# Performance work log

Hardware: AMD Instinct MI355X
Metric: run time of the kernel (lower is better)

The kernel has to match this reference:

```python
import jax, jax.numpy as jnp
import numpy as np

H, DQK, DV, DM, POS = 8, 64, 64, 768, 64

def _rel_basis(l, n):
    # Enformer central-mask relative position basis: [l, l, n]
    pos = jnp.arange(l)
    distance = pos[None, :] - pos[:, None]              # [l, l] int
    half = n // 2
    pow_rate = jnp.exp(jnp.log(jnp.asarray((l + 1) / 2.0, jnp.float32)) / half)
    center_widths = pow_rate ** jnp.arange(1, half + 1, dtype=jnp.float32)  # [half]
    unsigned = (jnp.abs(distance)[:, :, None].astype(jnp.float32) <= center_widths)
    signed = jnp.sign(distance)[:, :, None] * unsigned
    return jnp.concatenate([unsigned.astype(jnp.float32), signed.astype(jnp.float32)], axis=-1)

def setup_inputs() -> dict:
    key = jax.random.key(0)
    ks = jax.random.split(key, 9)
    b, l = 2, 1024
    x = jax.random.normal(ks[0], (b, l, DM), jnp.float32)
    # torch Linear weights: [out, in]
    Wq = jax.random.normal(ks[1], (H * DQK, DM), jnp.float32) * (1.0 / np.sqrt(DM))
    Wk = jax.random.normal(ks[2], (H * DQK, DM), jnp.float32) * (1.0 / np.sqrt(DM))
    Wv = jax.random.normal(ks[3], (H * DV, DM), jnp.float32) * (1.0 / np.sqrt(DM))
    Wo = jax.random.normal(ks[4], (DM, H * DV), jnp.float32) * (1.0 / np.sqrt(H * DV))
    bo = jnp.zeros((DM,), jnp.float32)
    u_bias = jax.random.normal(ks[5], (H, DQK), jnp.float32) * np.sqrt(2.0 / DQK)
    v_bias = jax.random.normal(ks[6], (H, DQK), jnp.float32) * np.sqrt(2.0 / DQK)
    w_pos = jax.random.normal(ks[7], (H, DQK, POS), jnp.float32) * np.sqrt(2.0 / POS)
    return {"x": x, "Wq": Wq, "Wk": Wk, "Wv": Wv, "Wo": Wo, "bo": bo,
            "u_bias": u_bias, "v_bias": v_bias, "w_pos": w_pos}

def reference(x, Wq, Wk, Wv, Wo, bo, u_bias, v_bias, w_pos):
    b, l, _ = x.shape
    q = (x @ Wq.T).reshape(b, l, H, DQK)
    k = (x @ Wk.T).reshape(b, l, H, DQK)
    v = (x @ Wv.T).reshape(b, l, H, DV)
    basis = _rel_basis(l, POS)                           # [l, l, n]
    scale = 1.0 / np.sqrt(DQK)
    # qr_term: einsum('bihd,hdn,ijn->bhij') factored to avoid [b,h,l,l,d]
    qw = jnp.einsum('bihd,hdn->bhin', q, w_pos)          # [b,h,l,n]
    qr = jnp.einsum('bhin,ijn->bhij', qw, basis)
    uk = jnp.einsum('hd,bjhd->bhj', u_bias, k)[:, :, None, :]
    vw = jnp.einsum('hd,hdn->hn', v_bias, w_pos)
    vr = jnp.einsum('hn,ijn->hij', vw, basis)[None]      # [1,h,l,l]
    bias = (qr + uk + vr) * scale
    scores = jnp.einsum('bihd,bjhd->bhij', q, k) * scale + bias
    attn = jax.nn.softmax(scores, axis=-1)
    out = jnp.einsum('bhij,bjhd->bihd', attn, v).reshape(b, l, H * DV)
    return out @ Wo.T + bo
```

## Files before the change

### kernel.cpp

```cpp
#include <hip/hip_runtime.h>

#define LSEQ 1024
#define NB   2
#define NH   8
#define DD   64
#define DMOD 768

using bf16x8 = __attribute__((ext_vector_type(8))) short;
using f32x4  = __attribute__((ext_vector_type(4))) float;

__device__ inline unsigned short f2bf(float f) {
    union { float f; unsigned u; } v; v.f = f;
    unsigned r = v.u + 0x7FFFu + ((v.u >> 16) & 1u);
    return (unsigned short)(r >> 16);
}
__device__ inline float bf2f(unsigned short u) {
    union { unsigned u; float f; } v; v.u = ((unsigned)u) << 16;
    return v.f;
}

__global__ __launch_bounds__(256) void pack_all(
    const float4* __restrict__ x,  const float4* __restrict__ wq,
    const float4* __restrict__ wk, const float4* __restrict__ wv,
    const float4* __restrict__ wo,
    ushort4* __restrict__ xb, ushort4* __restrict__ wqb, ushort4* __restrict__ wkb,
    ushort4* __restrict__ wvb, ushort4* __restrict__ wob)
{
    int i = blockIdx.x * 256 + threadIdx.x;
    const float4* src; ushort4* dst; int off;
    if (i < 393216)      { src = x;  dst = xb;  off = i; }
    else if (i < 491520) { src = wq; dst = wqb; off = i - 393216; }
    else if (i < 589824) { src = wk; dst = wkb; off = i - 491520; }
    else if (i < 688128) { src = wv; dst = wvb; off = i - 589824; }
    else                 { src = wo; dst = wob; off = i - 688128; }
    float4 v = src[off];
    ushort4 o;
    o.x = f2bf(v.x); o.y = f2bf(v.y); o.z = f2bf(v.z); o.w = f2bf(v.w);
    dst[off] = o;
}

__global__ void setup_kernel(const float* __restrict__ v_bias,
                             const float* __restrict__ w_pos,
                             float* __restrict__ vsfx,
                             unsigned char* __restrict__ cls_g)
{
    __shared__ float w_s[32];
    __shared__ float vw_s[8][64];
    __shared__ int cmin_s[1024];
    int tid = threadIdx.x;
    if (tid < 32) {
        float pr = expf(logf(512.5f) / 32.0f);
        w_s[tid] = powf(pr, (float)(tid + 1));
    }
    __syncthreads();
    for (int d = tid; d < 1024; d += 256) {
        float fd = (float)d;
        int cm = 32;
        for (int c = 31; c >= 0; --c) if (fd <= w_s[c]) cm = c;
        cmin_s[d] = cm;
    }
    for (int idx = tid; idx < 512; idx += 256) {
        int hh = idx >> 6, n = idx & 63;
        float s = 0.f;
        for (int d = 0; d < 64; ++d)
            s += v_bias[hh * 64 + d] * w_pos[(hh * 64 + d) * 64 + n];
        vw_s[hh][n] = s;
    }
    __syncthreads();
    for (int idx = tid; idx < 512; idx += 256) {
        int hh = idx >> 6, n = idx & 63;
        float s = 0.f;
        if (n < 32) { for (int c = n;      c < 32; ++c) s += vw_s[hh][c]; }
        else        { for (int c = n - 32; c < 32; ++c) s += vw_s[hh][32 + c]; }
        vsfx[idx] = s;
    }
    for (int d2 = tid; d2 < 2048; d2 += 256) {
        int dd = d2 - 1023;
        int ad = dd < 0 ? -dd : dd; if (ad > 1023) ad = 1023;
        int t = (dd < 0) ? 0 : ((dd == 0) ? 1 : 2);
        cls_g[d2] = (unsigned char)(t * 33 + cmin_s[ad]);
    }
}

__global__ __launch_bounds__(256) void gemm_qkv(
    const unsigned short* __restrict__ X, const unsigned short* __restrict__ W,
    const float* __restrict__ ub,
    unsigned short* __restrict__ Qb, unsigned short* __restrict__ Kb,
    unsigned short* __restrict__ Vtb)
{
    __shared__ unsigned short Xs[64][40];
    __shared__ unsigned short Wsm[64][40];
    __shared__ unsigned short Ct[64][72];

    int tid = threadIdx.x;
    int w = tid >> 6, lane = tid & 63, l15 = lane & 15, q = lane >> 4;
    int M0 = blockIdx.y * 64, N0 = blockIdx.x * 64;
    int rs = tid >> 2, seg = tid & 3;

    f32x4 acc[4] = {};
    for (int k0 = 0; k0 < 768; k0 += 32) {
        uint4 xv = *(const uint4*)(X + (size_t)(M0 + rs) * 768 + k0 + seg * 8);
        uint4 wv = *(const uint4*)(W + (size_t)(N0 + rs) * 768 + k0 + seg * 8);
        *(uint4*)&Xs[rs][seg * 8]  = xv;
        *(uint4*)&Wsm[rs][seg * 8] = wv;
        __syncthreads();
        bf16x8 a = *(bf16x8*)&Xs[w * 16 + l15][q * 8];
#pragma unroll
        for (int ct = 0; ct < 4; ++ct) {
            bf16x8 bfr = *(bf16x8*)&Wsm[ct * 16 + l15][q * 8];
            acc[ct] = __builtin_amdgcn_mfma_f32_16x16x32_bf16(a, bfr, acc[ct], 0, 0, 0);
        }
        __syncthreads();
    }

    if (N0 < 1024) {
        int isQ = (N0 < 512);
#pragma unroll
        for (int ct = 0; ct < 4; ++ct) {
            float u0 = isQ ? ub[N0 + ct * 16 + l15] : 0.f;
            float sc = isQ ? 0.125f : 1.0f;
#pragma unroll
            for (int r = 0; r < 4; ++r)
                Ct[w * 16 + q * 4 + r][ct * 16 + l15] = f2bf((acc[ct][r] + u0) * sc);
        }
        __syncthreads();
        int Nh = isQ ? N0 : (N0 - 512);
        unsigned short* out = isQ ? Qb : Kb;
        size_t base = ((size_t)((M0 >> 10) * 8 + (Nh >> 6)) * 1024 + (M0 & 1023)) * 64;
#pragma unroll
        for (int it = 0; it < 2; ++it) {
            int idx = tid + it * 256;
            int row = idx >> 3, sg = idx & 7;
            *(uint4*)(out + base + (size_t)row * 64 + sg * 8) = *(uint4*)&Ct[row][sg * 8];
        }
    } else {
#pragma unroll
        for (int ct = 0; ct < 4; ++ct) {
            ushort4 pk;
            pk.x = f2bf(acc[ct][0]); pk.y = f2bf(acc[ct][1]);
            pk.z = f2bf(acc[ct][2]); pk.w = f2bf(acc[ct][3]);
            *(ushort4*)&Ct[ct * 16 + l15][w * 16 + q * 4] = pk;
        }
        __syncthreads();
        size_t base = ((size_t)((M0 >> 10) * 8 + ((N0 - 1024) >> 6))) * 65536;
        int j0 = M0 & 1023;
#pragma unroll
        for (int it = 0; it < 2; ++it) {
            int idx = tid + it * 256;
            int d = idx >> 3, sg = idx & 7;
            *(uint4*)(Vtb + base + (size_t)d * 1024 + j0 + sg * 8) = *(uint4*)&Ct[d][sg * 8];
        }
    }
}

__global__ __launch_bounds__(256) void gemm_o(
    const unsigned short* __restrict__ X, const unsigned short* __restrict__ W,
    const float* __restrict__ bias, float* __restrict__ out)
{
    __shared__ unsigned short Xs[64][40];
    __shared__ unsigned short Wsm[64][40];
    __shared__ float Ctf[64][72];

    int tid = threadIdx.x;
    int w = tid >> 6, lane = tid & 63, l15 = lane & 15, q = lane >> 4;
    int M0 = blockIdx.y * 64, N0 = blockIdx.x * 64;
    int rs = tid >> 2, seg = tid & 3;

    f32x4 acc[4] = {};
    for (int k0 = 0; k0 < 512; k0 += 32) {
        uint4 xv = *(const uint4*)(X + (size_t)(M0 + rs) * 512 + k0 + seg * 8);
        uint4 wv = *(const uint4*)(W + (size_t)(N0 + rs) * 512 + k0 + seg * 8);
        *(uint4*)&Xs[rs][seg * 8]  = xv;
        *(uint4*)&Wsm[rs][seg * 8] = wv;
        __syncthreads();
        bf16x8 a = *(bf16x8*)&Xs[w * 16 + l15][q * 8];
#pragma unroll
        for (int ct = 0; ct < 4; ++ct) {
            bf16x8 bfr = *(bf16x8*)&Wsm[ct * 16 + l15][q * 8];
            acc[ct] = __builtin_amdgcn_mfma_f32_16x16x32_bf16(a, bfr, acc[ct], 0, 0, 0);
        }
        __syncthreads();
    }
#pragma unroll
    for (int ct = 0; ct < 4; ++ct) {
        float bv = bias[N0 + ct * 16 + l15];
#pragma unroll
        for (int r = 0; r < 4; ++r)
            Ctf[w * 16 + q * 4 + r][ct * 16 + l15] = acc[ct][r] + bv;
    }
    __syncthreads();
#pragma unroll
    for (int it = 0; it < 4; ++it) {
        int idx = tid + it * 256;
        int row = idx >> 4, sg = idx & 15;
        *(float4*)(out + (size_t)(M0 + row) * 768 + N0 + sg * 4) = *(float4*)&Ctf[row][sg * 4];
    }
}

__global__ __launch_bounds__(256) void qw_sfx_kernel(
    const unsigned short* __restrict__ qb,
    const float* __restrict__ w_pos,
    const float* __restrict__ ub,
    float* __restrict__ qsfx)
{
    __shared__ float wps[64][64];
    __shared__ float qs[4][64];
    __shared__ float qw[4][64];
    int h = blockIdx.y, b = blockIdx.z;
    int i0 = blockIdx.x * 4;
    int n = threadIdx.x, r = threadIdx.y;
    int tid = r * 64 + n;
    for (int idx = tid; idx < 4096; idx += 256)
        wps[idx >> 6][idx & 63] = w_pos[h * 4096 + idx];
    qs[r][n] = bf2f(qb[((size_t)(b * 8 + h) * 1024 + i0 + r) * 64 + n]) * 8.0f
               - ub[h * 64 + n];
    __syncthreads();
    float acc = 0.f;
#pragma unroll 8
    for (int d = 0; d < 64; ++d) acc += qs[r][d] * wps[d][n];
    qw[r][n] = acc;
    __syncthreads();
    float s = 0.f;
    if (n < 32) { for (int c = 31; c >= n;      --c) s += qw[r][c]; }
    else        { for (int c = 31; c >= n - 32; --c) s += qw[r][32 + c]; }
    qsfx[((size_t)(b * 8 + h) * 1024 + i0 + r) * 64 + n] = s;
}

__global__ __launch_bounds__(256, 4) void attn_mfma(
    const unsigned short* __restrict__ Qbf,
    const unsigned short* __restrict__ Kbf,
    const unsigned short* __restrict__ Vt,
    const float* __restrict__ qsfx, const float* __restrict__ vsfx,
    const unsigned char* __restrict__ cls_g,
    unsigned short* __restrict__ ao)
{
    __shared__ float biasT[16 * 99];
    __shared__ unsigned char cls[2048];
    __shared__ unsigned short Pl[4][16][76];
    __shared__ float Obuf[4][64][17];
    __shared__ float lbuf[4][16];

    int tid = threadIdx.x;
    int b = blockIdx.z, h = blockIdx.y, bh = b * 8 + h;
    int i0 = blockIdx.x * 16;
    int w = tid >> 6, lane = tid & 63, l15 = lane & 15, q = lane >> 4;

    for (int idx = tid; idx < 512; idx += 256)
        ((unsigned int*)cls)[idx] = ((const unsigned int*)cls_g)[idx];
    for (int idx = tid; idx < 528; idx += 256) {
        int il = idx / 33, c = idx - il * 33;
        float up = 0.f, sp = 0.f;
        if (c < 32) {
            const float* qs = qsfx + ((size_t)bh * 1024 + i0 + il) * 64;
            const float* vs = vsfx + h * 64;
            up = (qs[c] + vs[c]) * 0.125f;
            sp = (qs[32 + c] + vs[32 + c]) * 0.125f;
        }
        float* bt = biasT + il * 99;
        bt[c]      = up - sp;
        bt[33 + c] = up;
        bt[66 + c] = up + sp;
    }
    __syncthreads();

    int ig = i0 + l15;
    const unsigned short* qrow = Qbf + ((size_t)bh * 1024 + ig) * 64;
    bf16x8 qf0 = *(const bf16x8*)(qrow + q * 8);
    bf16x8 qf1 = *(const bf16x8*)(qrow + 32 + q * 8);
    const unsigned short* Kbase = Kbf + (size_t)bh * 65536;
    const unsigned short* Vbase = Vt  + (size_t)bh * 65536;
    const float* btrow = biasT + l15 * 99;
    int clsoff = 1023 - ig;

    f32x4 Oacc[4] = {};
    float lsum = 0.f;

    for (int jt = 0; jt < 4; ++jt) {
        int jb = w * 256 + jt * 64;
        f32x4 st[4];
#pragma unroll
        for (int ct = 0; ct < 4; ++ct) {
            const unsigned short* krow = Kbase + (size_t)(jb + ct * 16 + l15) * 64;
            bf16x8 ka0 = *(const bf16x8*)(krow + q * 8);
            bf16x8 ka1 = *(const bf16x8*)(krow + 32 + q * 8);
            f32x4 a = {};
            a = __builtin_amdgcn_mfma_f32_16x16x32_bf16(ka0, qf0, a, 0, 0, 0);
            a = __builtin_amdgcn_mfma_f32_16x16x32_bf16(ka1, qf1, a, 0, 0, 0);
            st[ct] = a;
        }
#pragma unroll
        for (int ct = 0; ct < 4; ++ct) {
            int d2b = jb + ct * 16 + q * 4 + clsoff;
            float pv[4];
#pragma unroll
            for (int r = 0; r < 4; ++r) {
                float s = st[ct][r] + btrow[cls[d2b + r]];
                float p = __expf(s);
                lsum += p;
                pv[r] = p;
            }
            ushort4 pk;
            pk.x = f2bf(pv[0]); pk.y = f2bf(pv[1]);
            pk.z = f2bf(pv[2]); pk.w = f2bf(pv[3]);
            *(ushort4*)&Pl[w][l15][ct * 16 + q * 4] = pk;
        }
#pragma unroll
        for (int ks = 0; ks < 2; ++ks) {
            bf16x8 pb = *(const bf16x8*)&Pl[w][l15][ks * 32 + q * 8];
#pragma unroll
            for (int dt = 0; dt < 4; ++dt) {
                bf16x8 va = *(const bf16x8*)(Vbase + (size_t)(dt * 16 + l15) * 1024
                                             + jb + ks * 32 + q * 8);
                Oacc[dt] = __builtin_amdgcn_mfma_f32_16x16x32_bf16(va, pb, Oacc[dt], 0, 0, 0);
            }
        }
    }

    lsum += __shfl_xor(lsum, 16);
    lsum += __shfl_xor(lsum, 32);

#pragma unroll
    for (int dt = 0; dt < 4; ++dt)
#pragma unroll
        for (int r = 0; r < 4; ++r)
            Obuf[w][dt * 16 + q * 4 + r][l15] = Oacc[dt][r];
    if (lane < 16) lbuf[w][l15] = lsum;
    __syncthreads();

    for (int t2 = tid; t2 < 1024; t2 += 256) {
        int il = t2 >> 6, d = t2 & 63;
        float o = Obuf[0][d][il] + Obuf[1][d][il] + Obuf[2][d][il] + Obuf[3][d][il];
        float l = lbuf[0][il] + lbuf[1][il] + lbuf[2][il] + lbuf[3][il];
        ao[((size_t)(b * 1024 + i0 + il)) * 512 + h * 64 + d] = f2bf(o / l);
    }
}

extern "C" void kernel_launch(void* const* d_in, const int* in_sizes, int n_in,
                              void* d_out, int out_size, void* d_ws, size_t ws_size,
                              hipStream_t stream)
{
    const float* x      = (const float*)d_in[0];
    const float* Wq     = (const float*)d_in[1];
    const float* Wk     = (const float*)d_in[2];
    const float* Wv     = (const float*)d_in[3];
    const float* Wo     = (const float*)d_in[4];
    const float* bo     = (const float*)d_in[5];
    const float* u_bias = (const float*)d_in[6];
    const float* v_bias = (const float*)d_in[7];
    const float* w_pos  = (const float*)d_in[8];
    float* out = (float*)d_out;

    char* ws = (char*)d_ws;
    unsigned short* Xbf  = (unsigned short*)ws;            ws += 3145728;
    unsigned short* Wqkv = (unsigned short*)ws;            ws += 2359296;
    unsigned short* Wob  = (unsigned short*)ws;            ws += 786432;
    unsigned short* Qbf  = (unsigned short*)ws;            ws += 2097152;
    unsigned short* Kbf  = (unsigned short*)ws;            ws += 2097152;
    unsigned short* Vtb  = (unsigned short*)ws;            ws += 2097152;
    unsigned short* aob  = (unsigned short*)ws;            ws += 2097152;
    float*          qsfx = (float*)ws;                     ws += 4194304;
    float*          vsfx = (float*)ws;                     ws += 2048;
    unsigned char*  clsg = (unsigned char*)ws;             ws += 2048;

    pack_all<<<3072, 256, 0, stream>>>(
        (const float4*)x, (const float4*)Wq, (const float4*)Wk,
        (const float4*)Wv, (const float4*)Wo,
        (ushort4*)Xbf,
        (ushort4*)Wqkv, (ushort4*)Wqkv + 98304, (ushort4*)Wqkv + 196608,
        (ushort4*)Wob);

    setup_kernel<<<1, 256, 0, stream>>>(v_bias, w_pos, vsfx, clsg);

    gemm_qkv<<<dim3(24, 32), 256, 0, stream>>>(Xbf, Wqkv, u_bias, Qbf, Kbf, Vtb);

    qw_sfx_kernel<<<dim3(256, 8, 2), dim3(64, 4), 0, stream>>>(Qbf, w_pos, u_bias, qsfx);

    attn_mfma<<<dim3(64, 8, 2), 256, 0, stream>>>(
        Qbf, Kbf, Vtb, qsfx, vsfx, clsg, aob);

    gemm_o<<<dim3(12, 32), 256, 0, stream>>>(aob, Wob, bo, out);
}
```

Baseline: 165.7 us.

## Fuse q·w_pos suffix computation into QKV GEMM epilogue and merge setup into pack

The separate qw_sfx kernel is removed. Its q·w_pos projection is now computed with MFMA in the Q-tile epilogue of gemm_qkv from the bf16 Q already in shared memory, against a bf16 transposed copy of w_pos, and the suffix sums are written to qsfx there. Because the biased, scaled Q is used, the u_bias term is folded algebraically into a precomputed (v-u)·w_pos suffix table. The setup kernel also becomes an extra block of the pack kernel, which saves two launches. The cost is a serial suffix-sum loop and extra shared memory in the Q blocks, plus bf16 precision for the positional projection.

```diff
diff --git a/kernel.cpp b/kernel.cpp
--- a/kernel.cpp
+++ b/kernel.cpp
@@ -19,13 +19,68 @@
     return v.f;
 }
 
-__global__ __launch_bounds__(256) void pack_all(
+__global__ __launch_bounds__(256) void pack_setup(
     const float4* __restrict__ x,  const float4* __restrict__ wq,
     const float4* __restrict__ wk, const float4* __restrict__ wv,
     const float4* __restrict__ wo,
+    const float* __restrict__ u_bias, const float* __restrict__ v_bias,
+    const float* __restrict__ w_pos,
     ushort4* __restrict__ xb, ushort4* __restrict__ wqb, ushort4* __restrict__ wkb,
-    ushort4* __restrict__ wvb, ushort4* __restrict__ wob)
+    ushort4* __restrict__ wvb, ushort4* __restrict__ wob,
+    float* __restrict__ wsfx, unsigned char* __restrict__ cls_g,
+    unsigned short* __restrict__ wpt)
 {
+    if (blockIdx.x == 3072) {
+        __shared__ float w_s[32];
+        __shared__ float vw_s[8][64];
+        __shared__ float uw_s[8][64];
+        __shared__ int cmin_s[1024];
+        int tid = threadIdx.x;
+        if (tid < 32) {
+            float pr = expf(logf(512.5f) / 32.0f);
+            w_s[tid] = powf(pr, (float)(tid + 1));
+        }
+        __syncthreads();
+        for (int d = tid; d < 1024; d += 256) {
+            float fd = (float)d;
+            int cm = 32;
+            for (int c = 31; c >= 0; --c) if (fd <= w_s[c]) cm = c;
+            cmin_s[d] = cm;
+        }
+        for (int idx = tid; idx < 512; idx += 256) {
+            int hh = idx >> 6, n = idx & 63;
+            float vs = 0.f, us = 0.f;
+            for (int d = 0; d < 64; ++d) {
+                float wp = w_pos[(hh * 64 + d) * 64 + n];
+                vs += v_bias[hh * 64 + d] * wp;
+                us += u_bias[hh * 64 + d] * wp;
+            }
+            vw_s[hh][n] = vs;
+            uw_s[hh][n] = us;
+        }
+        __syncthreads();
+        for (int idx = tid; idx < 512; idx += 256) {
+            int hh = idx >> 6, n = idx & 63;
+            float vs = 0.f, us = 0.f;
+            if (n < 32) {
+                for (int c = n; c < 32; ++c) { vs += vw_s[hh][c]; us += uw_s[hh][c]; }
+            } else {
+                for (int c = n - 32; c < 32; ++c) { vs += vw_s[hh][32 + c]; us += uw_s[hh][32 + c]; }
+            }
+            wsfx[idx] = (vs - us) * 0.125f;
+        }
+        for (int d2 = tid; d2 < 2048; d2 += 256) {
+            int dd = d2 - 1023;
+            int ad = dd < 0 ? -dd : dd; if (ad > 1023) ad = 1023;
+            int t = (dd < 0) ? 0 : ((dd == 0) ? 1 : 2);
+            cls_g[d2] = (unsigned char)(t * 33 + cmin_s[ad]);
+        }
+        for (int idx = tid; idx < 32768; idx += 256) {
+            int hh = idx >> 12, n = (idx >> 6) & 63, d = idx & 63;
+            wpt[idx] = f2bf(w_pos[(hh * 64 + d) * 64 + n]);
+        }
+        return;
+    }
     int i = blockIdx.x * 256 + threadIdx.x;
     const float4* src; ushort4* dst; int off;
     if (i < 393216)      { src = x;  dst = xb;  off = i; }
@@ -39,63 +94,31 @@
     dst[off] = o;
 }
 
-__global__ void setup_kernel(const float* __restrict__ v_bias,
-                             const float* __restrict__ w_pos,
-                             float* __restrict__ vsfx,
-                             unsigned char* __restrict__ cls_g)
-{
-    __shared__ float w_s[32];
-    __shared__ float vw_s[8][64];
-    __shared__ int cmin_s[1024];
-    int tid = threadIdx.x;
-    if (tid < 32) {
-        float pr = expf(logf(512.5f) / 32.0f);
-        w_s[tid] = powf(pr, (float)(tid + 1));
-    }
-    __syncthreads();
-    for (int d = tid; d < 1024; d += 256) {
-        float fd = (float)d;
-        int cm = 32;
-        for (int c = 31; c >= 0; --c) if (fd <= w_s[c]) cm = c;
-        cmin_s[d] = cm;
-    }
-    for (int idx = tid; idx < 512; idx += 256) {
-        int hh = idx >> 6, n = idx & 63;
-        float s = 0.f;
-        for (int d = 0; d < 64; ++d)
-            s += v_bias[hh * 64 + d] * w_pos[(hh * 64 + d) * 64 + n];
-        vw_s[hh][n] = s;
-    }
-    __syncthreads();
-    for (int idx = tid; idx < 512; idx += 256) {
-        int hh = idx >> 6, n = idx & 63;
-        float s = 0.f;
-        if (n < 32) { for (int c = n;      c < 32; ++c) s += vw_s[hh][c]; }
-        else        { for (int c = n - 32; c < 32; ++c) s += vw_s[hh][32 + c]; }
-        vsfx[idx] = s;
-    }
-    for (int d2 = tid; d2 < 2048; d2 += 256) {
-        int dd = d2 - 1023;
-        int ad = dd < 0 ? -dd : dd; if (ad > 1023) ad = 1023;
-        int t = (dd < 0) ? 0 : ((dd == 0) ? 1 : 2);
-        cls_g[d2] = (unsigned char)(t * 33 + cmin_s[ad]);
-    }
-}
-
 __global__ __launch_bounds__(256) void gemm_qkv(
     const unsigned short* __restrict__ X, const unsigned short* __restrict__ W,
-    const float* __restrict__ ub,
+    const float* __restrict__ ub, const unsigned short* __restrict__ wpt,
     unsigned short* __restrict__ Qb, unsigned short* __restrict__ Kb,
-    unsigned short* __restrict__ Vtb)
+    unsigned short* __restrict__ Vtb, float* __restrict__ qsfx)
 {
     __shared__ unsigned short Xs[64][40];
     __shared__ unsigned short Wsm[64][40];
     __shared__ unsigned short Ct[64][72];
+    __shared__ unsigned short wpt_s[64][64];
+    __shared__ float qwf[64][68];
 
     int tid = threadIdx.x;
     int w = tid >> 6, lane = tid & 63, l15 = lane & 15, q = lane >> 4;
     int M0 = blockIdx.y * 64, N0 = blockIdx.x * 64;
     int rs = tid >> 2, seg = tid & 3;
+    int isQ = (N0 < 512);
+    int h = N0 >> 6;
+
+    if (isQ) {
+        const ushort4* src = (const ushort4*)(wpt + h * 4096);
+#pragma unroll
+        for (int t = 0; t < 4; ++t)
+            ((ushort4*)wpt_s)[tid * 4 + t] = src[tid * 4 + t];
+    }
 
     f32x4 acc[4] = {};
     for (int k0 = 0; k0 < 768; k0 += 32) {
@@ -114,7 +137,6 @@
     }
 
     if (N0 < 1024) {
-        int isQ = (N0 < 512);
 #pragma unroll
         for (int ct = 0; ct < 4; ++ct) {
             float u0 = isQ ? ub[N0 + ct * 16 + l15] : 0.f;
@@ -132,6 +154,33 @@
             int idx = tid + it * 256;
             int row = idx >> 3, sg = idx & 7;
             *(uint4*)(out + base + (size_t)row * 64 + sg * 8) = *(uint4*)&Ct[row][sg * 8];
+        }
+        if (isQ) {
+            bf16x8 a0 = *(bf16x8*)&Ct[w * 16 + l15][q * 8];
+            bf16x8 a1 = *(bf16x8*)&Ct[w * 16 + l15][32 + q * 8];
+#pragma unroll
+            for (int ct = 0; ct < 4; ++ct) {
+                bf16x8 b0 = *(bf16x8*)&wpt_s[ct * 16 + l15][q * 8];
+                bf16x8 b1 = *(bf16x8*)&wpt_s[ct * 16 + l15][32 + q * 8];
+                f32x4 a = {};
+                a = __builtin_amdgcn_mfma_f32_16x16x32_bf16(a0, b0, a, 0, 0, 0);
+                a = __builtin_amdgcn_mfma_f32_16x16x32_bf16(a1, b1, a, 0, 0, 0);
+#pragma unroll
+                for (int r = 0; r < 4; ++r)
+                    qwf[w * 16 + q * 4 + r][ct * 16 + l15] = a[r];
+            }
+            __syncthreads();
+            int n = tid & 63, rg = tid >> 6;
+            int nn = n & 31, cbase = n & 32;
+            int b = M0 >> 10, bh = b * 8 + h, i0 = M0 & 1023;
+            float* qout = qsfx + ((size_t)bh * 1024 + i0) * 64 + n;
+#pragma unroll
+            for (int rr = 0; rr < 16; ++rr) {
+                int row = rg * 16 + rr;
+                float s = 0.f;
+                for (int c = 31; c >= nn; --c) s += qwf[row][cbase + c];
+                qout[(size_t)row * 64] = s;
+            }
         }
     } else {
 #pragma unroll
@@ -197,40 +246,12 @@
     }
 }
 
-__global__ __launch_bounds__(256) void qw_sfx_kernel(
-    const unsigned short* __restrict__ qb,
-    const float* __restrict__ w_pos,
-    const float* __restrict__ ub,
-    float* __restrict__ qsfx)
-{
-    __shared__ float wps[64][64];
-    __shared__ float qs[4][64];
-    __shared__ float qw[4][64];
-    int h = blockIdx.y, b = blockIdx.z;
-    int i0 = blockIdx.x * 4;
-    int n = threadIdx.x, r = threadIdx.y;
-    int tid = r * 64 + n;
-    for (int idx = tid; idx < 4096; idx += 256)
-        wps[idx >> 6][idx & 63] = w_pos[h * 4096 + idx];
-    qs[r][n] = bf2f(qb[((size_t)(b * 8 + h) * 1024 + i0 + r) * 64 + n]) * 8.0f
-               - ub[h * 64 + n];
-    __syncthreads();
-    float acc = 0.f;
-#pragma unroll 8
-    for (int d = 0; d < 64; ++d) acc += qs[r][d] * wps[d][n];
-    qw[r][n] = acc;
-    __syncthreads();
-    float s = 0.f;
-    if (n < 32) { for (int c = 31; c >= n;      --c) s += qw[r][c]; }
-    else        { for (int c = 31; c >= n - 32; --c) s += qw[r][32 + c]; }
-    qsfx[((size_t)(b * 8 + h) * 1024 + i0 + r) * 64 + n] = s;
-}
-
 __global__ __launch_bounds__(256, 4) void attn_mfma(
     const unsigned short* __restrict__ Qbf,
     const unsigned short* __restrict__ Kbf,
     const unsigned short* __restrict__ Vt,
-    const float* __restrict__ qsfx, const float* __restrict__ vsfx,
+    const float* __restrict__ qsfx,
+    const float* __restrict__ wsfx,
     const unsigned char* __restrict__ cls_g,
     unsigned short* __restrict__ ao)
 {
@@ -252,9 +273,9 @@
         float up = 0.f, sp = 0.f;
         if (c < 32) {
             const float* qs = qsfx + ((size_t)bh * 1024 + i0 + il) * 64;
-            const float* vs = vsfx + h * 64;
-            up = (qs[c] + vs[c]) * 0.125f;
-            sp = (qs[32 + c] + vs[32 + c]) * 0.125f;
+            const float* vs = wsfx + h * 64;
+            up = qs[c] + vs[c];
+            sp = qs[32 + c] + vs[32 + c];
         }
         float* bt = biasT + il * 99;
         bt[c]      = up - sp;
@@ -359,24 +380,24 @@
     unsigned short* Vtb  = (unsigned short*)ws;            ws += 2097152;
     unsigned short* aob  = (unsigned short*)ws;            ws += 2097152;
     float*          qsfx = (float*)ws;                     ws += 4194304;
-    float*          vsfx = (float*)ws;                     ws += 2048;
+    float*          wsfx = (float*)ws;                     ws += 2048;
     unsigned char*  clsg = (unsigned char*)ws;             ws += 2048;
-
-    pack_all<<<3072, 256, 0, stream>>>(
+    unsigned short* wpt  = (unsigned short*)ws;            ws += 65536;
+
+    pack_setup<<<3073, 256, 0, stream>>>(
         (const float4*)x, (const float4*)Wq, (const float4*)Wk,
         (const float4*)Wv, (const float4*)Wo,
+        u_bias, v_bias, w_pos,
         (ushort4*)Xbf,
         (ushort4*)Wqkv, (ushort4*)Wqkv + 98304, (ushort4*)Wqkv + 196608,
-        (ushort4*)Wob);
-
-    setup_kernel<<<1, 256, 0, stream>>>(v_bias, w_pos, vsfx, clsg);
-
-    gemm_qkv<<<dim3(24, 32), 256, 0, stream>>>(Xbf, Wqkv, u_bias, Qbf, Kbf, Vtb);
-
-    qw_sfx_kernel<<<dim3(256, 8, 2), dim3(64, 4), 0, stream>>>(Qbf, w_pos, u_bias, qsfx);
+        (ushort4*)Wob,
+        wsfx, clsg, wpt);
+
+    gemm_qkv<<<dim3(24, 32), 256, 0, stream>>>(Xbf, Wqkv, u_bias, wpt,
+                                               Qbf, Kbf, Vtb, qsfx);
 
     attn_mfma<<<dim3(64, 8, 2), 256, 0, stream>>>(
-        Qbf, Kbf, Vtb, qsfx, vsfx, clsg, aob);
+        Qbf, Kbf, Vtb, qsfx, wsfx, clsg, aob);
 
     gemm_o<<<dim3(12, 32), 256, 0, stream>>>(aob, Wob, bo, out);
 }
```

Measured after the change: 181.2 us. 1.09x slower.
